# Kernel optimization log

Hardware: AMD Instinct MI355X
Metric: run time of the kernel (lower is better)

Reference implementation:

```python
import jax, jax.numpy as jnp
import numpy as np

N = 100000          # nodes
E = 1600000         # edges (before self-loops)
F_IN = 512          # num_node_features
H1, C1 = 8, 8       # layer-1 heads, per-head channels
NUM_CLASSES = 40
NEG_SLOPE = 0.2     # PyG GATConv default


def setup_inputs() -> dict:
    key = jax.random.key(0)
    ks = jax.random.split(key, 10)
    x = jax.random.normal(ks[0], (N, F_IN), jnp.float32)
    edge_index = jax.random.randint(ks[1], (2, E), 0, N, dtype=jnp.int64)
    # Glorot-ish scaled params (matches PyG init scale qualitatively)
    W1 = jax.random.normal(ks[2], (F_IN, H1 * C1), jnp.float32) / np.sqrt(F_IN)
    a_src1 = jax.random.normal(ks[3], (H1, C1), jnp.float32) / np.sqrt(C1)
    a_dst1 = jax.random.normal(ks[4], (H1, C1), jnp.float32) / np.sqrt(C1)
    b1 = jnp.zeros((H1 * C1,), jnp.float32)
    W2 = jax.random.normal(ks[5], (H1 * C1, NUM_CLASSES), jnp.float32) / np.sqrt(H1 * C1)
    a_src2 = jax.random.normal(ks[6], (1, NUM_CLASSES), jnp.float32) / np.sqrt(NUM_CLASSES)
    a_dst2 = jax.random.normal(ks[7], (1, NUM_CLASSES), jnp.float32) / np.sqrt(NUM_CLASSES)
    b2 = jnp.zeros((NUM_CLASSES,), jnp.float32)
    return {"x": x, "edge_index": edge_index, "W1": W1, "a_src1": a_src1,
            "a_dst1": a_dst1, "b1": b1, "W2": W2, "a_src2": a_src2,
            "a_dst2": a_dst2, "b2": b2}


def gat_layer(x, src, dst, W, a_s, a_d, b, concat):
    """PyG GATConv (eval mode: dropout=0). src -> dst messages, softmax over dst."""
    heads, ch = a_s.shape
    n = x.shape[0]
    h = (x @ W).reshape(n, heads, ch)                      # [N,H,C]
    alpha_s = jnp.einsum('nhc,hc->nh', h, a_s)             # [N,H]
    alpha_d = jnp.einsum('nhc,hc->nh', h, a_d)
    e = jax.nn.leaky_relu(alpha_s[src] + alpha_d[dst], NEG_SLOPE)   # [E,H]
    # segment softmax over incoming edges of each dst node
    m = jax.ops.segment_max(e, dst, num_segments=n)        # [N,H]
    p = jnp.exp(e - m[dst])
    s = jax.ops.segment_sum(p, dst, num_segments=n)
    alpha = p / (s[dst] + 1e-16)                           # [E,H]
    out = jax.ops.segment_sum(h[src] * alpha[..., None], dst, num_segments=n)  # [N,H,C]
    out = out.reshape(n, heads * ch) if concat else out.mean(axis=1)
    return out + b


def reference(x, edge_index, W1, a_src1, a_dst1, b1, W2, a_src2, a_dst2, b2):
    n = x.shape[0]
    loops = jnp.arange(n, dtype=edge_index.dtype)
    src = jnp.concatenate([edge_index[0], loops])          # add self-loops (PyG default)
    dst = jnp.concatenate([edge_index[1], loops])
    h = gat_layer(x, src, dst, W1, a_src1, a_dst1, b1, concat=True)
    h = jax.nn.elu(h)
    out = gat_layer(h, src, dst, W2, a_src2, a_dst2, b2, concat=False)
    return jax.nn.log_softmax(out, axis=1)
```

## Files before the change

kernel.cpp:

```cpp
#include <hip/hip_runtime.h>
#include <hip/hip_bf16.h>

#define F_IN 512
#define HC1 64
#define NH1 8
#define NC 40
#define NEG_SLOPE 0.2f
#define SCAN_CHUNK 2048
#define RADIX_EPB 4096
#define MAXNB 512

__global__ void detect_i64(const int* __restrict__ ei, int* __restrict__ flag, int n_check) {
    __shared__ int found;
    if (threadIdx.x == 0) found = 0;
    __syncthreads();
    for (int i = threadIdx.x; i < n_check; i += 256) {
        if (ei[2 * i + 1] != 0) atomicOr(&found, 1);
    }
    __syncthreads();
    if (threadIdx.x == 0) *flag = (found == 0) ? 1 : 0;
}

__global__ void hist_kernel(const int* __restrict__ ei, const int* __restrict__ flag,
                            int* __restrict__ deg, int E) {
    int e = blockIdx.x * 256 + threadIdx.x;
    if (e >= E) return;
    int f = *flag;
    int d = f ? ei[2 * (E + e)] : ei[E + e];
    atomicAdd(&deg[d], 1);
}

__global__ __launch_bounds__(256) void scan1(const int* __restrict__ deg, int* __restrict__ rowptr,
                                             int* __restrict__ bsums, int n) {
    __shared__ int sbuf[256];
    int tid = threadIdx.x;
    int base = blockIdx.x * SCAN_CHUNK + tid * 8;
    int v[8];
#pragma unroll
    for (int j = 0; j < 8; j++) { int idx = base + j; v[j] = (idx < n) ? deg[idx] : 0; }
    int tsum = 0;
#pragma unroll
    for (int j = 0; j < 8; j++) tsum += v[j];
    sbuf[tid] = tsum;
    __syncthreads();
    for (int off = 1; off < 256; off <<= 1) {
        int t = (tid >= off) ? sbuf[tid - off] : 0;
        __syncthreads();
        sbuf[tid] += t;
        __syncthreads();
    }
    int run = sbuf[tid] - tsum;
#pragma unroll
    for (int j = 0; j < 8; j++) {
        run += v[j];
        int idx = base + j;
        if (idx < n) rowptr[1 + idx] = run;
    }
    if (tid == 255) bsums[blockIdx.x] = sbuf[255];
}

__global__ void scan2(int* __restrict__ bsums, int nb) {
    int lane = threadIdx.x & 63;
    int v = (lane < nb) ? bsums[lane] : 0;
    int orig = v;
    for (int off = 1; off < 64; off <<= 1) {
        int t = __shfl_up(v, (unsigned)off, 64);
        if (lane >= off) v += t;
    }
    if (lane < nb) bsums[lane] = v - orig;
}

__global__ void scan3(const int* __restrict__ deg, int* __restrict__ rowptr,
                      int* __restrict__ bcur, const int* __restrict__ bsums, int n) {
    int i = blockIdx.x * 256 + threadIdx.x;
    if (i >= n) return;
    int off = bsums[i >> 11];
    int incl = rowptr[1 + i] + off;
    rowptr[1 + i] = incl;
    if ((i & 255) == 0) bcur[i >> 8] = incl - deg[i];
    if (i == 0) rowptr[0] = 0;
}

__global__ __launch_bounds__(256) void scatter1(const int* __restrict__ ei, const int* __restrict__ flag,
                                                int* __restrict__ bcur, int2* __restrict__ pairs,
                                                int E, int NB) {
    __shared__ int cnt[MAXNB];
    __shared__ int gb[MAXNB];
    int tid = threadIdx.x;
    for (int i = tid; i < NB; i += 256) cnt[i] = 0;
    __syncthreads();
    int f = *flag;
    int base = blockIdx.x * RADIX_EPB;
    int sv[16], dv[16], rv[16];
#pragma unroll
    for (int i = 0; i < 16; i++) {
        int e = base + i * 256 + tid;
        if (e < E) {
            int s, d;
            if (f) { s = ei[2 * e]; d = ei[2 * (E + e)]; }
            else   { s = ei[e];     d = ei[E + e]; }
            sv[i] = s; dv[i] = d;
            rv[i] = atomicAdd(&cnt[d >> 8], 1);
        }
    }
    __syncthreads();
    for (int i = tid; i < NB; i += 256) {
        int c = cnt[i];
        gb[i] = c ? atomicAdd(&bcur[i], c) : 0;
    }
    __syncthreads();
#pragma unroll
    for (int i = 0; i < 16; i++) {
        int e = base + i * 256 + tid;
        if (e < E) {
            int pos = gb[dv[i] >> 8] + rv[i];
            pairs[pos] = make_int2(sv[i], dv[i]);
        }
    }
}

__global__ __launch_bounds__(256) void scatter2(const int2* __restrict__ pairs,
                                                const int* __restrict__ rowptr,
                                                int* __restrict__ col, int Nn) {
    __shared__ int cur[256];
    int b = blockIdx.x;
    int node0 = b << 8;
    int tid = threadIdx.x;
    int nlast = min(node0 + 256, Nn);
    if (node0 + tid < nlast) cur[tid] = rowptr[node0 + tid];
    __syncthreads();
    int jb = rowptr[node0];
    int je = rowptr[nlast];
    for (int j = jb + tid; j < je; j += 256) {
        int2 pr = pairs[j];
        int pos = atomicAdd(&cur[pr.y - node0], 1);
        col[pos] = pr.x;
    }
}

__global__ __launch_bounds__(256) void gemm1(const float* __restrict__ x, const float* __restrict__ W,
                                             float* __restrict__ h1, int Nn) {
    __shared__ __align__(16) float xsT[32][68];
    __shared__ __align__(16) float ws[32][64];
    int tid = threadIdx.x;
    int m0 = blockIdx.x * 64;
    int tx = tid & 15, ty = tid >> 4;
    float acc[4][4] = {{0.f}};

    int lr = tid >> 2;
    int lk = (tid & 3) * 8;
    int wrow = tid >> 3;
    int wcol = (tid & 7) * 8;
    bool rowok = (m0 + lr) < Nn;
    const float* xrow = x + (size_t)(m0 + lr) * F_IN;

    for (int k0 = 0; k0 < F_IN; k0 += 32) {
        float4 a0 = make_float4(0.f, 0.f, 0.f, 0.f), a1 = a0;
        if (rowok) {
            a0 = *(const float4*)(xrow + k0 + lk);
            a1 = *(const float4*)(xrow + k0 + lk + 4);
        }
        float4 b0 = *(const float4*)(W + (size_t)(k0 + wrow) * HC1 + wcol);
        float4 b1 = *(const float4*)(W + (size_t)(k0 + wrow) * HC1 + wcol + 4);
        __syncthreads();
        xsT[lk + 0][lr] = a0.x; xsT[lk + 1][lr] = a0.y;
        xsT[lk + 2][lr] = a0.z; xsT[lk + 3][lr] = a0.w;
        xsT[lk + 4][lr] = a1.x; xsT[lk + 5][lr] = a1.y;
        xsT[lk + 6][lr] = a1.z; xsT[lk + 7][lr] = a1.w;
        *(float4*)&ws[wrow][wcol] = b0;
        *(float4*)&ws[wrow][wcol + 4] = b1;
        __syncthreads();
#pragma unroll
        for (int kk = 0; kk < 32; ++kk) {
            float4 av = *(const float4*)&xsT[kk][ty * 4];
            float4 bv = *(const float4*)&ws[kk][tx * 4];
            float aa[4] = {av.x, av.y, av.z, av.w};
            float bb[4] = {bv.x, bv.y, bv.z, bv.w};
#pragma unroll
            for (int i = 0; i < 4; i++)
#pragma unroll
                for (int j = 0; j < 4; j++) acc[i][j] += aa[i] * bb[j];
        }
    }
#pragma unroll
    for (int i = 0; i < 4; i++) {
        int r = m0 + ty * 4 + i;
        if (r < Nn) {
            *(float4*)(h1 + (size_t)r * HC1 + tx * 4) =
                make_float4(acc[i][0], acc[i][1], acc[i][2], acc[i][3]);
        }
    }
}

__global__ void alpha1_kernel(const float* __restrict__ h1, const float* __restrict__ a_s,
                              const float* __restrict__ a_d, float* __restrict__ as1,
                              float* __restrict__ ad1, int Nn) {
    int idx = blockIdx.x * 256 + threadIdx.x;
    if (idx >= Nn * NH1) return;
    int h = idx & 7;
    const float* hp = h1 + (size_t)(idx >> 3) * HC1 + h * 8;
    float s = 0.f, d = 0.f;
#pragma unroll
    for (int c = 0; c < 8; c++) {
        float v = hp[c];
        s += v * a_s[h * 8 + c];
        d += v * a_d[h * 8 + c];
    }
    as1[idx] = s;
    ad1[idx] = d;
}

__device__ __forceinline__ float lrelu(float e) { return e > 0.f ? e : NEG_SLOPE * e; }

__global__ __launch_bounds__(256) void agg1(const float* __restrict__ h1, const float* __restrict__ as1,
                                            const float* __restrict__ ad1, const int* __restrict__ rowptr,
                                            const int* __restrict__ col, const float* __restrict__ b1,
                                            float* __restrict__ h2, int Nn) {
    __shared__ float pbuf[4][NH1 * 68];
    int w = threadIdx.x >> 6;
    int wave = (blockIdx.x * 256 + threadIdx.x) >> 6;
    int lane = threadIdx.x & 63;
    if (wave >= Nn) return;
    int d = wave;
    int jb = rowptr[d], je = rowptr[d + 1];
    const float4* as4 = (const float4*)as1;
    const float4* ad4 = (const float4*)ad1;

    float4 sd0 = as4[d * 2], sd1 = as4[d * 2 + 1];
    float4 dd0 = ad4[d * 2], dd1 = ad4[d * 2 + 1];
    float ad[8] = {dd0.x, dd0.y, dd0.z, dd0.w, dd1.x, dd1.y, dd1.z, dd1.w};
    float sv[8] = {sd0.x, sd0.y, sd0.z, sd0.w, sd1.x, sd1.y, sd1.z, sd1.w};
    float e0[8];
#pragma unroll
    for (int h = 0; h < NH1; h++) e0[h] = lrelu(sv[h] + ad[h]);

    int myh = lane >> 3;
    float acc = h1[(size_t)d * HC1 + lane];
    float ssum = 1.0f;
    float* pb = pbuf[w];

    for (int c0 = jb; c0 < je; c0 += 64) {
        int nc = min(64, je - c0);
        int srcv = d;
        if (lane < nc) srcv = col[c0 + lane];
        float4 a0 = as4[srcv * 2], a1 = as4[srcv * 2 + 1];
        float ev[8] = {a0.x, a0.y, a0.z, a0.w, a1.x, a1.y, a1.z, a1.w};
#pragma unroll
        for (int h = 0; h < NH1; h++)
            pb[h * 68 + lane] = __expf(lrelu(ev[h] + ad[h]) - e0[h]);

        int jj = 0;
        for (; jj + 3 < nc; jj += 4) {
            int s0 = __shfl(srcv, jj, 64), s1 = __shfl(srcv, jj + 1, 64);
            int s2 = __shfl(srcv, jj + 2, 64), s3 = __shfl(srcv, jj + 3, 64);
            float p0 = pb[myh * 68 + jj],     p1 = pb[myh * 68 + jj + 1];
            float p2 = pb[myh * 68 + jj + 2], p3 = pb[myh * 68 + jj + 3];
            float g0 = h1[(size_t)s0 * HC1 + lane];
            float g1 = h1[(size_t)s1 * HC1 + lane];
            float g2 = h1[(size_t)s2 * HC1 + lane];
            float g3 = h1[(size_t)s3 * HC1 + lane];
            ssum += (p0 + p1) + (p2 + p3);
            acc += p0 * g0 + p1 * g1 + p2 * g2 + p3 * g3;
        }
        for (; jj < nc; jj++) {
            int s0 = __shfl(srcv, jj, 64);
            float p0 = pb[myh * 68 + jj];
            ssum += p0;
            acc += p0 * h1[(size_t)s0 * HC1 + lane];
        }
    }
    float o = acc / (ssum + 1e-16f) + b1[lane];
    o = o > 0.f ? o : __expf(o) - 1.0f;
    h2[(size_t)d * HC1 + lane] = o;
}

__global__ __launch_bounds__(256) void gemm2(const float* __restrict__ h2, const float* __restrict__ W2,
                                             const float* __restrict__ av_in, const float* __restrict__ dv_in,
                                             float* __restrict__ g, float* __restrict__ as2,
                                             float* __restrict__ ad2, int Nn) {
    __shared__ float W2s[HC1 * NC];
    __shared__ float hrow[4][HC1];
    __shared__ float avec[NC], dvec[NC];
    int tid = threadIdx.x;
    for (int i = tid; i < HC1 * NC; i += 256) W2s[i] = W2[i];
    if (tid < NC) { avec[tid] = av_in[tid]; dvec[tid] = dv_in[tid]; }
    int w = tid >> 6, lane = tid & 63;
    int n = blockIdx.x * 4 + w;
    float hv = 0.f;
    if (n < Nn) hv = h2[(size_t)n * HC1 + lane];
    hrow[w][lane] = hv;
    __syncthreads();
    float acc = 0.f;
    bool act = (n < Nn) && (lane < NC);
    if (act) {
#pragma unroll
        for (int k = 0; k < HC1; k++) acc += hrow[w][k] * W2s[k * NC + lane];
        g[(size_t)n * NC + lane] = acc;
    }
    float va = act ? acc * avec[lane] : 0.f;
    float vd = act ? acc * dvec[lane] : 0.f;
    for (int off = 32; off; off >>= 1) {
        va += __shfl_xor(va, off, 64);
        vd += __shfl_xor(vd, off, 64);
    }
    if (n < Nn && lane == 0) { as2[n] = va; ad2[n] = vd; }
}

__global__ __launch_bounds__(256) void agg2(const float* __restrict__ g, const float* __restrict__ as2,
                                            const float* __restrict__ ad2, const int* __restrict__ rowptr,
                                            const int* __restrict__ col, const float* __restrict__ b2,
                                            float* __restrict__ out, int Nn) {
    __shared__ float pbuf[4][64];
    int w = threadIdx.x >> 6;
    int wave = (blockIdx.x * 256 + threadIdx.x) >> 6;
    int lane = threadIdx.x & 63;
    if (wave >= Nn) return;
    int d = wave;
    int jb = rowptr[d], je = rowptr[d + 1];
    float adv = ad2[d];
    float e0 = lrelu(as2[d] + adv);
    float acc = (lane < NC) ? g[(size_t)d * NC + lane] : 0.f;
    float ssum = 1.0f;
    float* pb = pbuf[w];

    for (int c0 = jb; c0 < je; c0 += 64) {
        int nc = min(64, je - c0);
        int srcv = d;
        if (lane < nc) srcv = col[c0 + lane];
        pb[lane] = __expf(lrelu(as2[srcv] + adv) - e0);

        int jj = 0;
        for (; jj + 3 < nc; jj += 4) {
            int s0 = __shfl(srcv, jj, 64), s1 = __shfl(srcv, jj + 1, 64);
            int s2 = __shfl(srcv, jj + 2, 64), s3 = __shfl(srcv, jj + 3, 64);
            float p0 = pb[jj], p1 = pb[jj + 1], p2 = pb[jj + 2], p3 = pb[jj + 3];
            float g0 = 0.f, g1 = 0.f, g2 = 0.f, g3 = 0.f;
            if (lane < NC) {
                g0 = g[(size_t)s0 * NC + lane];
                g1 = g[(size_t)s1 * NC + lane];
                g2 = g[(size_t)s2 * NC + lane];
                g3 = g[(size_t)s3 * NC + lane];
            }
            ssum += (p0 + p1) + (p2 + p3);
            acc += p0 * g0 + p1 * g1 + p2 * g2 + p3 * g3;
        }
        for (; jj < nc; jj++) {
            int s0 = __shfl(srcv, jj, 64);
            float p0 = pb[jj];
            ssum += p0;
            if (lane < NC) acc += p0 * g[(size_t)s0 * NC + lane];
        }
    }
    float o = acc / (ssum + 1e-16f) + ((lane < NC) ? b2[lane] : 0.f);
    float vm = (lane < NC) ? o : -1e30f;
#pragma unroll
    for (int off = 32; off; off >>= 1) vm = fmaxf(vm, __shfl_xor(vm, off, 64));
    float ex = (lane < NC) ? __expf(o - vm) : 0.f;
#pragma unroll
    for (int off = 32; off; off >>= 1) ex += __shfl_xor(ex, off, 64);
    float lsm = o - vm - __logf(ex);
    if (lane < NC) out[(size_t)d * NC + lane] = lsm;
}

extern "C" void kernel_launch(void* const* d_in, const int* in_sizes, int n_in,
                              void* d_out, int out_size, void* d_ws, size_t ws_size,
                              hipStream_t stream) {
    const float* x      = (const float*)d_in[0];
    const int*   ei     = (const int*)d_in[1];
    const float* W1     = (const float*)d_in[2];
    const float* a_src1 = (const float*)d_in[3];
    const float* a_dst1 = (const float*)d_in[4];
    const float* b1     = (const float*)d_in[5];
    const float* W2     = (const float*)d_in[6];
    const float* a_src2 = (const float*)d_in[7];
    const float* a_dst2 = (const float*)d_in[8];
    const float* b2     = (const float*)d_in[9];
    float* out = (float*)d_out;

    const int N = in_sizes[0] / F_IN;
    const int E = in_sizes[1] / 2;
    const int NB = (N + 255) >> 8;

    char* p = (char*)d_ws;
    auto alloc = [&](size_t bytes) -> void* {
        void* r = (void*)p;
        p += (bytes + 255) & ~(size_t)255;
        return r;
    };
    int2* pairs = (int2*)alloc((size_t)E * 8);
    int* deg    = (int*)alloc((size_t)N * 4);
    int* rowptr = (int*)alloc(((size_t)N + 1) * 4);
    int* bcur   = (int*)alloc((size_t)MAXNB * 4);
    int* bsums  = (int*)alloc(64 * 4);
    int* flag   = (int*)alloc(256);
    int* col    = (int*)alloc((size_t)E * 4);
    float* h1   = (float*)alloc((size_t)N * HC1 * 4);
    float* as1  = (float*)alloc((size_t)N * NH1 * 4);
    float* ad1  = (float*)alloc((size_t)N * NH1 * 4);
    float* h2   = (float*)alloc((size_t)N * HC1 * 4);
    float* g    = h1;
    float* as2  = as1;
    float* ad2  = ad1;

    hipMemsetAsync(deg, 0, (size_t)N * 4, stream);
    detect_i64<<<1, 256, 0, stream>>>(ei, flag, 4096);
    int ge = (E + 255) / 256;
    hist_kernel<<<ge, 256, 0, stream>>>(ei, flag, deg, E);
    int nb = (N + SCAN_CHUNK - 1) / SCAN_CHUNK;
    scan1<<<nb, 256, 0, stream>>>(deg, rowptr, bsums, N);
    scan2<<<1, 64, 0, stream>>>(bsums, nb);
    scan3<<<(N + 255) / 256, 256, 0, stream>>>(deg, rowptr, bcur, bsums, N);
    scatter1<<<(E + RADIX_EPB - 1) / RADIX_EPB, 256, 0, stream>>>(ei, flag, bcur, pairs, E, NB);
    scatter2<<<NB, 256, 0, stream>>>(pairs, rowptr, col, N);

    gemm1<<<(N + 63) / 64, 256, 0, stream>>>(x, W1, h1, N);
    alpha1_kernel<<<(N * NH1 + 255) / 256, 256, 0, stream>>>(h1, a_src1, a_dst1, as1, ad1, N);
    agg1<<<(N + 3) / 4, 256, 0, stream>>>(h1, as1, ad1, rowptr, col, b1, h2, N);

    gemm2<<<(N + 3) / 4, 256, 0, stream>>>(h2, W2, a_src2, a_dst2, g, as2, ad2, N);
    agg2<<<(N + 3) / 4, 256, 0, stream>>>(g, as2, ad2, rowptr, col, b2, out, N);
}
```

Baseline: 669.4 us.

## Use bf16 MFMA for layer-1 GEMM, fuse alpha, store h1 as bf16

Layer-1 projection now converts x and W tiles to bf16 in shared memory and computes them with 16x16x32 bf16 MFMA instructions instead of scalar FP32 FMAs. The attention-score computation (alpha1) is folded into the GEMM epilogue, which removes a separate kernel and its re-read of h1. h1 is stored as bf16, which halves the bytes of the per-edge gathers in agg1. In exchange, inputs and h1 lose precision to bf16, which may move outputs relative to the FP32 reference.

```diff
diff --git a/kernel.cpp b/kernel.cpp
--- a/kernel.cpp
+++ b/kernel.cpp
@@ -9,6 +9,19 @@
 #define SCAN_CHUNK 2048
 #define RADIX_EPB 4096
 #define MAXNB 512
+
+typedef short bf16x8 __attribute__((ext_vector_type(8)));
+typedef float f32x4 __attribute__((ext_vector_type(4)));
+
+static __device__ __forceinline__ unsigned short f2b(float f) {
+    __hip_bfloat16 h = __float2bfloat16(f);
+    return *(unsigned short*)&h;
+}
+static __device__ __forceinline__ float b2f(unsigned short u) {
+    union { unsigned int i; float f; } v;
+    v.i = ((unsigned int)u) << 16;
+    return v.f;
+}
 
 __global__ void detect_i64(const int* __restrict__ ei, int* __restrict__ flag, int n_check) {
     __shared__ int found;
@@ -139,80 +152,93 @@
 }
 
 __global__ __launch_bounds__(256) void gemm1(const float* __restrict__ x, const float* __restrict__ W,
-                                             float* __restrict__ h1, int Nn) {
-    __shared__ __align__(16) float xsT[32][68];
-    __shared__ __align__(16) float ws[32][64];
+                                             const float* __restrict__ a_s, const float* __restrict__ a_d,
+                                             unsigned short* __restrict__ h1, float* __restrict__ as1,
+                                             float* __restrict__ ad1, int Nn) {
+    __shared__ unsigned short xs[64][72];
+    __shared__ unsigned short wsT[64][72];
     int tid = threadIdx.x;
     int m0 = blockIdx.x * 64;
-    int tx = tid & 15, ty = tid >> 4;
-    float acc[4][4] = {{0.f}};
-
-    int lr = tid >> 2;
-    int lk = (tid & 3) * 8;
-    int wrow = tid >> 3;
-    int wcol = (tid & 7) * 8;
-    bool rowok = (m0 + lr) < Nn;
-    const float* xrow = x + (size_t)(m0 + lr) * F_IN;
-
-    for (int k0 = 0; k0 < F_IN; k0 += 32) {
-        float4 a0 = make_float4(0.f, 0.f, 0.f, 0.f), a1 = a0;
-        if (rowok) {
-            a0 = *(const float4*)(xrow + k0 + lk);
-            a1 = *(const float4*)(xrow + k0 + lk + 4);
-        }
-        float4 b0 = *(const float4*)(W + (size_t)(k0 + wrow) * HC1 + wcol);
-        float4 b1 = *(const float4*)(W + (size_t)(k0 + wrow) * HC1 + wcol + 4);
+    int w = tid >> 6, lane = tid & 63;
+    int quad = lane >> 4, mr = lane & 15;
+    f32x4 acc[4];
+#pragma unroll
+    for (int i = 0; i < 4; i++) acc[i] = (f32x4){0.f, 0.f, 0.f, 0.f};
+
+    int lrow = tid >> 4;
+    int lf4 = tid & 15;
+
+    for (int k0 = 0; k0 < F_IN; k0 += 64) {
+        float4 xv[4], wv[4];
+#pragma unroll
+        for (int i = 0; i < 4; i++) {
+            int row = i * 16 + lrow;
+            xv[i] = (m0 + row < Nn) ? *(const float4*)(x + (size_t)(m0 + row) * F_IN + k0 + lf4 * 4)
+                                    : make_float4(0.f, 0.f, 0.f, 0.f);
+            wv[i] = *(const float4*)(W + (size_t)(k0 + row) * HC1 + lf4 * 4);
+        }
         __syncthreads();
-        xsT[lk + 0][lr] = a0.x; xsT[lk + 1][lr] = a0.y;
-        xsT[lk + 2][lr] = a0.z; xsT[lk + 3][lr] = a0.w;
-        xsT[lk + 4][lr] = a1.x; xsT[lk + 5][lr] = a1.y;
-        xsT[lk + 6][lr] = a1.z; xsT[lk + 7][lr] = a1.w;
-        *(float4*)&ws[wrow][wcol] = b0;
-        *(float4*)&ws[wrow][wcol + 4] = b1;
+#pragma unroll
+        for (int i = 0; i < 4; i++) {
+            int row = i * 16 + lrow;
+            xs[row][lf4 * 4 + 0] = f2b(xv[i].x);
+            xs[row][lf4 * 4 + 1] = f2b(xv[i].y);
+            xs[row][lf4 * 4 + 2] = f2b(xv[i].z);
+            xs[row][lf4 * 4 + 3] = f2b(xv[i].w);
+            wsT[lf4 * 4 + 0][row] = f2b(wv[i].x);
+            wsT[lf4 * 4 + 1][row] = f2b(wv[i].y);
+            wsT[lf4 * 4 + 2][row] = f2b(wv[i].z);
+            wsT[lf4 * 4 + 3][row] = f2b(wv[i].w);
+        }
         __syncthreads();
 #pragma unroll
-        for (int kk = 0; kk < 32; ++kk) {
-            float4 av = *(const float4*)&xsT[kk][ty * 4];
-            float4 bv = *(const float4*)&ws[kk][tx * 4];
-            float aa[4] = {av.x, av.y, av.z, av.w};
-            float bb[4] = {bv.x, bv.y, bv.z, bv.w};
-#pragma unroll
-            for (int i = 0; i < 4; i++)
-#pragma unroll
-                for (int j = 0; j < 4; j++) acc[i][j] += aa[i] * bb[j];
-        }
-    }
-#pragma unroll
-    for (int i = 0; i < 4; i++) {
-        int r = m0 + ty * 4 + i;
-        if (r < Nn) {
-            *(float4*)(h1 + (size_t)r * HC1 + tx * 4) =
-                make_float4(acc[i][0], acc[i][1], acc[i][2], acc[i][3]);
-        }
-    }
-}
-
-__global__ void alpha1_kernel(const float* __restrict__ h1, const float* __restrict__ a_s,
-                              const float* __restrict__ a_d, float* __restrict__ as1,
-                              float* __restrict__ ad1, int Nn) {
-    int idx = blockIdx.x * 256 + threadIdx.x;
-    if (idx >= Nn * NH1) return;
-    int h = idx & 7;
-    const float* hp = h1 + (size_t)(idx >> 3) * HC1 + h * 8;
-    float s = 0.f, d = 0.f;
-#pragma unroll
-    for (int c = 0; c < 8; c++) {
-        float v = hp[c];
-        s += v * a_s[h * 8 + c];
-        d += v * a_d[h * 8 + c];
-    }
-    as1[idx] = s;
-    ad1[idx] = d;
+        for (int ks = 0; ks < 2; ks++) {
+            bf16x8 a = *(const bf16x8*)&xs[w * 16 + mr][ks * 32 + quad * 8];
+#pragma unroll
+            for (int nb = 0; nb < 4; nb++) {
+                bf16x8 b = *(const bf16x8*)&wsT[nb * 16 + mr][ks * 32 + quad * 8];
+                acc[nb] = __builtin_amdgcn_mfma_f32_16x16x32_bf16(a, b, acc[nb], 0, 0, 0);
+            }
+        }
+    }
+    __syncthreads();
+    unsigned short (*hs)[72] = xs;
+#pragma unroll
+    for (int nb = 0; nb < 4; nb++)
+#pragma unroll
+        for (int r = 0; r < 4; r++)
+            hs[w * 16 + quad * 4 + r][nb * 16 + mr] = f2b(acc[nb][r]);
+    __syncthreads();
+    {
+        int srow = tid >> 2, sseg = tid & 3;
+        if (m0 + srow < Nn) {
+            uint4 v0 = *(const uint4*)&hs[srow][sseg * 16];
+            uint4 v1 = *(const uint4*)&hs[srow][sseg * 16 + 8];
+            uint4* dst = (uint4*)(h1 + (size_t)(m0 + srow) * HC1 + sseg * 16);
+            dst[0] = v0;
+            dst[1] = v1;
+        }
+    }
+    for (int i = tid; i < 512; i += 256) {
+        int row = i >> 3, hh = i & 7;
+        if (m0 + row < Nn) {
+            float s = 0.f, d = 0.f;
+#pragma unroll
+            for (int c = 0; c < 8; c++) {
+                float v = b2f(hs[row][hh * 8 + c]);
+                s += v * a_s[hh * 8 + c];
+                d += v * a_d[hh * 8 + c];
+            }
+            as1[(size_t)(m0 + row) * NH1 + hh] = s;
+            ad1[(size_t)(m0 + row) * NH1 + hh] = d;
+        }
+    }
 }
 
 __device__ __forceinline__ float lrelu(float e) { return e > 0.f ? e : NEG_SLOPE * e; }
 
-__global__ __launch_bounds__(256) void agg1(const float* __restrict__ h1, const float* __restrict__ as1,
+__global__ __launch_bounds__(256) void agg1(const unsigned short* __restrict__ h1,
+                                            const float* __restrict__ as1,
                                             const float* __restrict__ ad1, const int* __restrict__ rowptr,
                                             const int* __restrict__ col, const float* __restrict__ b1,
                                             float* __restrict__ h2, int Nn) {
@@ -235,7 +261,7 @@
     for (int h = 0; h < NH1; h++) e0[h] = lrelu(sv[h] + ad[h]);
 
     int myh = lane >> 3;
-    float acc = h1[(size_t)d * HC1 + lane];
+    float acc = b2f(h1[(size_t)d * HC1 + lane]);
     float ssum = 1.0f;
     float* pb = pbuf[w];
 
@@ -255,10 +281,10 @@
             int s2 = __shfl(srcv, jj + 2, 64), s3 = __shfl(srcv, jj + 3, 64);
             float p0 = pb[myh * 68 + jj],     p1 = pb[myh * 68 + jj + 1];
             float p2 = pb[myh * 68 + jj + 2], p3 = pb[myh * 68 + jj + 3];
-            float g0 = h1[(size_t)s0 * HC1 + lane];
-            float g1 = h1[(size_t)s1 * HC1 + lane];
-            float g2 = h1[(size_t)s2 * HC1 + lane];
-            float g3 = h1[(size_t)s3 * HC1 + lane];
+            float g0 = b2f(h1[(size_t)s0 * HC1 + lane]);
+            float g1 = b2f(h1[(size_t)s1 * HC1 + lane]);
+            float g2 = b2f(h1[(size_t)s2 * HC1 + lane]);
+            float g3 = b2f(h1[(size_t)s3 * HC1 + lane]);
             ssum += (p0 + p1) + (p2 + p3);
             acc += p0 * g0 + p1 * g1 + p2 * g2 + p3 * g3;
         }
@@ -266,7 +292,7 @@
             int s0 = __shfl(srcv, jj, 64);
             float p0 = pb[myh * 68 + jj];
             ssum += p0;
-            acc += p0 * h1[(size_t)s0 * HC1 + lane];
+            acc += p0 * b2f(h1[(size_t)s0 * HC1 + lane]);
         }
     }
     float o = acc / (ssum + 1e-16f) + b1[lane];
@@ -394,11 +420,11 @@
     int* bsums  = (int*)alloc(64 * 4);
     int* flag   = (int*)alloc(256);
     int* col    = (int*)alloc((size_t)E * 4);
-    float* h1   = (float*)alloc((size_t)N * HC1 * 4);
+    unsigned short* h1 = (unsigned short*)alloc((size_t)N * HC1 * 4);
     float* as1  = (float*)alloc((size_t)N * NH1 * 4);
     float* ad1  = (float*)alloc((size_t)N * NH1 * 4);
     float* h2   = (float*)alloc((size_t)N * HC1 * 4);
-    float* g    = h1;
+    float* g    = (float*)h1;
     float* as2  = as1;
     float* ad2  = ad1;
 
@@ -413,8 +439,7 @@
     scatter1<<<(E + RADIX_EPB - 1) / RADIX_EPB, 256, 0, stream>>>(ei, flag, bcur, pairs, E, NB);
     scatter2<<<NB, 256, 0, stream>>>(pairs, rowptr, col, N);
 
-    gemm1<<<(N + 63) / 64, 256, 0, stream>>>(x, W1, h1, N);
-    alpha1_kernel<<<(N * NH1 + 255) / 256, 256, 0, stream>>>(h1, a_src1, a_dst1, as1, ad1, N);
+    gemm1<<<(N + 63) / 64, 256, 0, stream>>>(x, W1, a_src1, a_dst1, h1, as1, ad1, N);
     agg1<<<(N + 3) / 4, 256, 0, stream>>>(h1, as1, ad1, rowptr, col, b1, h2, N);
 
     gemm2<<<(N + 3) / 4, 256, 0, stream>>>(h2, W2, a_src2, a_dst2, g, as2, ad2, N);
```

After: 639.1 us. 4.5% less time.
